# Kernel optimization log

Measured on AMD Instinct MI355X. Metric: run time of the kernel, lower is better.

The kernel has to match this reference:

```python
import jax, jax.numpy as jnp
import numpy as np

N_USERS = 100_000
N_ITEMS = 200_000
N_EDGES = 1_000_000
D = 64        # in_size == every layer_size
L = 3         # number of NGCF layers
B = 4096      # BPR batch
SLOPE = 0.2   # LeakyReLU negative slope
EPS = 1e-12   # F.normalize eps


def setup_inputs() -> dict:
    key = jax.random.key(0)
    ks = jax.random.split(key, 11)
    s = 1.0 / np.sqrt(D)  # xavier-ish scale
    return dict(
        user_feat=jax.random.normal(ks[0], (N_USERS, D), jnp.float32) * s,
        item_feat=jax.random.normal(ks[1], (N_ITEMS, D), jnp.float32) * s,
        W1=jax.random.normal(ks[2], (L, D, D), jnp.float32) * s,
        b1=jnp.zeros((L, D), jnp.float32),
        W2=jax.random.normal(ks[3], (L, D, D), jnp.float32) * s,
        b2=jnp.zeros((L, D), jnp.float32),
        edge_src=jax.random.randint(ks[4], (N_EDGES,), 0, N_USERS),
        edge_dst=jax.random.randint(ks[5], (N_EDGES,), 0, N_ITEMS),
        users=jax.random.randint(ks[6], (B,), 0, N_USERS),
        pos_items=jax.random.randint(ks[7], (B,), 0, N_ITEMS),
        neg_items=jax.random.randint(ks[8], (B,), 0, N_ITEMS),
    )


def _act_norm(h):
    # LeakyReLU(0.2) -> (dropout=identity, eval) -> row-wise L2 normalize
    h = jax.nn.leaky_relu(h, SLOPE)
    n = jnp.linalg.norm(h, axis=1, keepdims=True)
    return h / jnp.maximum(n, EPS)


def _ngcf_forward(user_feat, item_feat, W1, b1, W2, b2, edge_src, edge_dst):
    ones = jnp.ones((edge_src.shape[0],), user_feat.dtype)
    deg_u = jax.ops.segment_sum(ones, edge_src, num_segments=N_USERS)  # out-degree of users
    deg_i = jax.ops.segment_sum(ones, edge_dst, num_segments=N_ITEMS)  # in-degree of items
    norm = (deg_u[edge_src] * deg_i[edge_dst]) ** -0.5  # [E], same for both directions
    norm = norm[:, None]

    hu, hi = user_feat, item_feat
    u_embeds, i_embeds = [hu], [hi]
    for l in range(L):
        # per-edge elementwise product term (shared between both directions)
        p = hu[edge_src] * hi[edge_dst]            # [E, D]
        pw = p @ W2[l] + b2[l]                     # [E, D]
        # user -> item messages, summed per item
        m_i = norm * ((hu @ W1[l] + b1[l])[edge_src] + pw)
        # item -> user messages, summed per user
        m_u = norm * ((hi @ W1[l] + b1[l])[edge_dst] + pw)
        hi_new = jax.ops.segment_sum(m_i, edge_dst, num_segments=N_ITEMS)
        hu_new = jax.ops.segment_sum(m_u, edge_src, num_segments=N_USERS)
        hu, hi = _act_norm(hu_new), _act_norm(hi_new)
        u_embeds.append(hu)
        i_embeds.append(hi)

    user_embd = jnp.concatenate(u_embeds, axis=1)  # [N_USERS, D*(L+1)]
    item_embd = jnp.concatenate(i_embeds, axis=1)  # [N_ITEMS, D*(L+1)]
    return user_embd, item_embd


def reference(user_feat, item_feat, W1, b1, W2, b2,
              edge_src, edge_dst, users, pos_items, neg_items):
    user_embd, item_embd = _ngcf_forward(
        user_feat, item_feat, W1, b1, W2, b2, edge_src, edge_dst)
    return (user_embd[users], item_embd[pos_items], item_embd[neg_items])
```

## Files before the change

kernel.cpp:

```cpp
#include <hip/hip_runtime.h>

#define NU 100000
#define NI 200000
#define NE 1000000
#define NB 4096
#define CAP 16384
#define NBS 98
#define NBD 98
#define NTI (NI / 16)
#define NTU (NU / 16)
#define DBKT 64
#define CAPD 65536
#define NBI 196
#define NBU 98

typedef __attribute__((ext_vector_type(8))) short bf16x8;
typedef __attribute__((ext_vector_type(4))) float f32x4;
typedef __attribute__((ext_vector_type(8))) unsigned short u16x8;

static __device__ __forceinline__ short f2bf(float f) {
  unsigned u = __builtin_bit_cast(unsigned, f);
  unsigned r = (u + 0x7fffu + ((u >> 16) & 1u)) >> 16;
  return (short)r;
}
static __device__ __forceinline__ float bf2f(unsigned short u) {
  return __builtin_bit_cast(float, ((unsigned)u) << 16);
}

__global__ __launch_bounds__(256) void binA_kernel(const int* __restrict__ src,
                                                   const int* __restrict__ dst,
                                                   int* __restrict__ gcur_s,
                                                   int* __restrict__ gcur_d,
                                                   int2* __restrict__ temp_s,
                                                   int2* __restrict__ temp_d) {
  __shared__ int lh[128], lbase[128], lpos[128];
  const int dir = blockIdx.x >> 9;
  const int cb = blockIdx.x & 511;
  const int lo = (int)(((long long)NE * cb) >> 9);
  const int hi = (int)(((long long)NE * (cb + 1)) >> 9);
  const int* key = dir ? dst : src;
  const int* oth = dir ? src : dst;
  int* gcur = dir ? gcur_d : gcur_s;
  int2* temp = dir ? temp_d : temp_s;
  const int shift = dir ? 11 : 10;
  const int tid = threadIdx.x;
  if (tid < 128) lh[tid] = 0;
  __syncthreads();
  for (int e = lo + tid; e < hi; e += 256) atomicAdd(&lh[key[e] >> shift], 1);
  __syncthreads();
  if (tid < 128) {
    const int c = lh[tid];
    lbase[tid] = c ? atomicAdd(&gcur[tid], c) : 0;
    lpos[tid] = 0;
  }
  __syncthreads();
  for (int e = lo + tid; e < hi; e += 256) {
    const int k = key[e];
    const int b = k >> shift;
    const int p = lbase[b] + atomicAdd(&lpos[b], 1);
    temp[(size_t)b * CAP + p] = make_int2(k, oth[e]);
  }
}

__global__ void bktscan_kernel(const int* __restrict__ gcur_s, const int* __restrict__ gcur_d,
                               int* __restrict__ bktofs_s, int* __restrict__ bktofs_d,
                               int* __restrict__ ofs_u, int* __restrict__ ofs_i) {
  const int t = threadIdx.x;
  if (t == 0) {
    int a = 0;
    for (int i = 0; i < NBS; ++i) { bktofs_s[i] = a; a += gcur_s[i]; }
    bktofs_s[NBS] = a;
    ofs_u[NU] = NE;
  }
  if (t == 1) {
    int a = 0;
    for (int i = 0; i < NBD; ++i) { bktofs_d[i] = a; a += gcur_d[i]; }
    bktofs_d[NBD] = a;
    ofs_i[NI] = NE;
  }
}

__global__ __launch_bounds__(256) void placeB_kernel(const int2* __restrict__ temp_s,
                                                     const int2* __restrict__ temp_d,
                                                     const int* __restrict__ gcur_s,
                                                     const int* __restrict__ gcur_d,
                                                     const int* __restrict__ bktofs_s,
                                                     const int* __restrict__ bktofs_d,
                                                     int* __restrict__ ofs_u, int* __restrict__ ofs_i,
                                                     int* __restrict__ by_src, int* __restrict__ by_dst) {
  __shared__ int cnt[2048];
  __shared__ int exc[2048];
  __shared__ int wsum[256];
  const bool isdst = blockIdx.x >= NBS;
  const int b = isdst ? (int)blockIdx.x - NBS : (int)blockIdx.x;
  const int shift = isdst ? 11 : 10;
  const int nodelo = b << shift;
  const int n = isdst ? NI : NU;
  const int2* temp = (isdst ? temp_d : temp_s) + (size_t)b * CAP;
  const int ecnt = (isdst ? gcur_d : gcur_s)[b];
  const int bbase = (isdst ? bktofs_d : bktofs_s)[b];
  int* ofs = isdst ? ofs_i : ofs_u;
  int* by = isdst ? by_dst : by_src;
  const int tid = threadIdx.x;
  const int NN = 1 << shift;

  for (int j = tid; j < NN; j += 256) cnt[j] = 0;
  __syncthreads();
  for (int k = tid; k < ecnt; k += 256) atomicAdd(&cnt[temp[k].x - nodelo], 1);
  __syncthreads();
  const int per = NN >> 8;
  int s = 0;
  for (int j = 0; j < per; ++j) s += cnt[tid * per + j];
  wsum[tid] = s;
  __syncthreads();
  for (int off = 1; off < 256; off <<= 1) {
    int t2 = (tid >= off) ? wsum[tid - off] : 0;
    __syncthreads();
    wsum[tid] += t2;
    __syncthreads();
  }
  int run = wsum[tid] - s;
  for (int j = 0; j < per; ++j) {
    const int idx = tid * per + j;
    exc[idx] = run;
    run += cnt[idx];
  }
  __syncthreads();
  for (int j = tid; j < NN; j += 256) {
    const int node = nodelo + j;
    if (node < n) ofs[node] = bbase + exc[j];
  }
  __syncthreads();
  for (int j = tid; j < NN; j += 256) cnt[j] = exc[j];
  __syncthreads();
  for (int k = tid; k < ecnt; k += 256) {
    const int2 t2 = temp[k];
    const int p = bbase + atomicAdd(&cnt[t2.x - nodelo], 1);
    by[p] = t2.y;
  }
}

__global__ __launch_bounds__(256) void dbinA_kernel(const int* __restrict__ ofs_i,
                                                    const int* __restrict__ ofs_u,
                                                    int* __restrict__ dgcur,
                                                    int* __restrict__ arena_i,
                                                    int* __restrict__ arena_u) {
  __shared__ int lh[DBKT], lbase[DBKT], lpos[DBKT];
  const bool item = blockIdx.x < NBI;
  const int b = item ? (int)blockIdx.x : (int)blockIdx.x - NBI;
  const int n = item ? NI : NU;
  const int* ofs = item ? ofs_i : ofs_u;
  int* cur = dgcur + (item ? 0 : DBKT);
  int* arena = item ? arena_i : arena_u;
  const int nodelo = b << 10;
  const int nodehi = min(nodelo + 1024, n);
  const int tid = threadIdx.x;
  if (tid < DBKT) lh[tid] = 0;
  __syncthreads();
  for (int node = nodelo + tid; node < nodehi; node += 256)
    atomicAdd(&lh[min(ofs[node + 1] - ofs[node], DBKT - 1)], 1);
  __syncthreads();
  if (tid < DBKT) {
    const int c = lh[tid];
    lbase[tid] = c ? atomicAdd(&cur[tid], c) : 0;
    lpos[tid] = 0;
  }
  __syncthreads();
  for (int node = nodelo + tid; node < nodehi; node += 256) {
    const int d = min(ofs[node + 1] - ofs[node], DBKT - 1);
    const int p = lbase[d] + atomicAdd(&lpos[d], 1);
    arena[d * CAPD + p] = node;
  }
}

__global__ void dbktscan_kernel(const int* __restrict__ dgcur,
                                int* __restrict__ dofs, int* __restrict__ dedge,
                                int* __restrict__ ofs2_i, int* __restrict__ ofs2_u) {
  const int t = threadIdx.x;
  if (t == 0) {
    int a = 0, e = 0;
    for (int d = 0; d < DBKT; ++d) { dofs[d] = a; dedge[d] = e; a += dgcur[d]; e += dgcur[d] * d; }
    ofs2_i[NI] = NE;
  }
  if (t == 1) {
    int a = 0, e = 0;
    for (int d = 0; d < DBKT; ++d) {
      dofs[DBKT + d] = a; dedge[DBKT + d] = e;
      a += dgcur[DBKT + d]; e += dgcur[DBKT + d] * d;
    }
    ofs2_u[NU] = NE;
  }
}

__global__ __launch_bounds__(256) void dcompact_kernel(const int* __restrict__ dgcur,
                                                       const int* __restrict__ dofs,
                                                       const int* __restrict__ dedge,
                                                       const int* __restrict__ arena_i,
                                                       const int* __restrict__ arena_u,
                                                       int* __restrict__ perm_i, int* __restrict__ perm_u,
                                                       int* __restrict__ inv_i, int* __restrict__ inv_u,
                                                       int* __restrict__ ofs2_i, int* __restrict__ ofs2_u,
                                                       float* __restrict__ rs2_i, float* __restrict__ rs2_u,
                                                       float* __restrict__ srs2_i, float* __restrict__ srs2_u) {
  const int bk = blockIdx.x;
  const bool item = bk < DBKT;
  const int d = item ? bk : bk - DBKT;
  const int cnt = dgcur[bk];
  const int nodebase = dofs[bk];
  const int edgebase = dedge[bk];
  const int* arena = item ? arena_i : arena_u;
  int* perm = item ? perm_i : perm_u;
  int* inv = item ? inv_i : inv_u;
  int* ofs2 = item ? ofs2_i : ofs2_u;
  float* rs2 = item ? rs2_i : rs2_u;
  float* srs2 = item ? srs2_i : srs2_u;
  const float rsv = d ? rsqrtf((float)d) : 0.f;
  const float srsv = d ? sqrtf((float)d) : 0.f;
  for (int k = threadIdx.x; k < cnt; k += 256) {
    const int node = arena[d * CAPD + k];
    const int r = nodebase + k;
    perm[r] = node;
    inv[node] = r;
    ofs2[r] = edgebase + k * d;
    rs2[r] = rsv;
    srs2[r] = srsv;
  }
}

__global__ __launch_bounds__(256) void remapby_kernel(const int* __restrict__ ofs_i,
                                                      const int* __restrict__ ofs_u,
                                                      const int* __restrict__ ofs2_i,
                                                      const int* __restrict__ ofs2_u,
                                                      const int* __restrict__ perm_i,
                                                      const int* __restrict__ perm_u,
                                                      const int* __restrict__ inv_i,
                                                      const int* __restrict__ inv_u,
                                                      const int* __restrict__ by_dst,
                                                      const int* __restrict__ by_src,
                                                      int* __restrict__ by2_dst,
                                                      int* __restrict__ by2_src) {
  int r = blockIdx.x * 256 + threadIdx.x;
  if (r < NI) {
    const int lo2 = ofs2_i[r];
    const int d = ofs2_i[r + 1] - lo2;
    const int oo = ofs_i[perm_i[r]];
    for (int k = 0; k < d; ++k) by2_dst[lo2 + k] = inv_u[by_dst[oo + k]];
  } else if (r < NI + NU) {
    r -= NI;
    const int lo2 = ofs2_u[r];
    const int d = ofs2_u[r + 1] - lo2;
    const int oo = ofs_u[perm_u[r]];
    for (int k = 0; k < d; ++k) by2_src[lo2 + k] = inv_i[by_src[oo + k]];
  }
}

__global__ __launch_bounds__(256) void c_kernel(const int* __restrict__ ofs2_i,
                                                const int* __restrict__ ofs2_u,
                                                const int* __restrict__ by2_dst,
                                                const int* __restrict__ by2_src,
                                                const float* __restrict__ rs2_u,
                                                const float* __restrict__ rs2_i,
                                                float* __restrict__ c_i,
                                                float* __restrict__ c_u) {
  int r = blockIdx.x * 256 + threadIdx.x;
  if (r < NI) {
    const int lo = ofs2_i[r], hi = ofs2_i[r + 1];
    float s = 0.f;
    for (int k = lo; k < hi; ++k) s += rs2_u[by2_dst[k]];
    c_i[r] = rs2_i[r] * s;
  } else if (r < NI + NU) {
    r -= NI;
    const int lo = ofs2_u[r], hi = ofs2_u[r + 1];
    float s = 0.f;
    for (int k = lo; k < hi; ++k) s += rs2_i[by2_src[k]];
    c_u[r] = rs2_u[r] * s;
  }
}

__global__ __launch_bounds__(256) void conv_kernel(const float* __restrict__ uf,
                                                   const float* __restrict__ itf,
                                                   const int* __restrict__ perm_u,
                                                   const int* __restrict__ perm_i,
                                                   const float* __restrict__ rs2_u,
                                                   const float* __restrict__ rs2_i,
                                                   unsigned short* __restrict__ hsu,
                                                   unsigned short* __restrict__ hsi) {
  int i = blockIdx.x * 256 + threadIdx.x;
  const int n4u = NU * 16;
  const float* in;
  const int* perm;
  const float* rs;
  unsigned short* outp;
  int j;
  if (i < n4u) {
    in = uf; perm = perm_u; rs = rs2_u; outp = hsu; j = i;
  } else if (i < n4u + NI * 16) {
    in = itf; perm = perm_i; rs = rs2_i; outp = hsi; j = i - n4u;
  } else return;
  const int rnew = j >> 4;
  const int grp = j & 15;
  const float rsn = rs[rnew];
  float4 v = *(const float4*)&in[(size_t)perm[rnew] * 64 + grp * 4];
  ushort4 o;
  o.x = (unsigned short)f2bf(v.x * rsn);
  o.y = (unsigned short)f2bf(v.y * rsn);
  o.z = (unsigned short)f2bf(v.z * rsn);
  o.w = (unsigned short)f2bf(v.w * rsn);
  *(ushort4*)&outp[(size_t)j * 4] = o;
}

__global__ __launch_bounds__(256) void layer_fused_kernel(const int* __restrict__ ofs2_i,
                                                          const int* __restrict__ ofs2_u,
                                                          const int* __restrict__ by2_dst,
                                                          const int* __restrict__ by2_src,
                                                          const float* __restrict__ rs2_u,
                                                          const float* __restrict__ rs2_i,
                                                          const float* __restrict__ c_i,
                                                          const float* __restrict__ c_u,
                                                          const unsigned short* __restrict__ hsu,
                                                          const unsigned short* __restrict__ hsi,
                                                          const float* __restrict__ W1,
                                                          const float* __restrict__ b1,
                                                          const float* __restrict__ W2,
                                                          const float* __restrict__ b2,
                                                          unsigned short* __restrict__ hsi_new,
                                                          unsigned short* __restrict__ hsu_new) {
  __shared__ unsigned short wlds[8192];
  const int tid = threadIdx.x;
  const int lane = tid & 63;
  const int row16 = lane & 15;
  const int kg = lane >> 4;
  for (int ch = tid; ch < 1024; ch += 256) {
    const int w = ch >> 9;
    const int rem = ch & 511;
    const int nb = rem >> 7, kb = (rem >> 6) & 1, l2 = rem & 63;
    const int r16 = l2 & 15, kg2 = l2 >> 4;
    const float* W = w ? W2 : W1;
    unsigned short* dstp = &wlds[ch * 8];
#pragma unroll
    for (int j = 0; j < 8; ++j)
      dstp[j] = (unsigned short)f2bf(W[(kb * 32 + kg2 * 8 + j) * 64 + nb * 16 + r16]);
  }
  __syncthreads();

  float bsum[4];
#pragma unroll
  for (int nb = 0; nb < 4; ++nb) bsum[nb] = b1[nb * 16 + row16] + b2[nb * 16 + row16];

  const int wid = (blockIdx.x * 256 + tid) >> 6;
  const int nwaves = (gridDim.x * 256) >> 6;

  for (int t = wid; t < NTI + NTU; t += nwaves) {
    const bool item = t < NTI;
    const int tt = item ? t : t - NTI;
    const int* ofs = item ? ofs2_i : ofs2_u;
    const int* pay = item ? by2_dst : by2_src;
    const float* rsw = item ? rs2_i : rs2_u;
    const float* cc = item ? c_i : c_u;
    const unsigned short* hs = item ? hsu : hsi;
    const unsigned short* hsown = item ? hsi : hsu;
    unsigned short* hsnew = item ? hsi_new : hsu_new;
    const int r0 = tt * 16;
    const int node = r0 + row16;

    const int lo = ofs[node], hiE = ofs[node + 1];
    int rounds = (hiE - lo + 3) >> 2;
#pragma unroll
    for (int m = 1; m < 16; m <<= 1) rounds = max(rounds, __shfl_xor(rounds, m));

    float a0[8] = {0.f, 0.f, 0.f, 0.f, 0.f, 0.f, 0.f, 0.f};
    float a1[8] = {0.f, 0.f, 0.f, 0.f, 0.f, 0.f, 0.f, 0.f};
    for (int rd = 0; rd < rounds; ++rd) {
      const int i0 = lo + rd * 4;
      int nb4[4];
      float wt[4];
#pragma unroll
      for (int s = 0; s < 4; ++s) {
        const int idx = i0 + s;
        nb4[s] = pay[min(idx, NE - 1)];
        wt[s] = (idx < hiE) ? 1.f : 0.f;
      }
      u16x8 h0[4], h1[4];
#pragma unroll
      for (int s = 0; s < 4; ++s) {
        const unsigned short* hp = hs + (size_t)nb4[s] * 64 + kg * 8;
        h0[s] = *(const u16x8*)hp;
        h1[s] = *(const u16x8*)(hp + 32);
      }
#pragma unroll
      for (int s = 0; s < 4; ++s)
#pragma unroll
        for (int j = 0; j < 8; ++j) {
          a0[j] += wt[s] * bf2f(h0[s][j]);
          a1[j] += wt[s] * bf2f(h1[s][j]);
        }
    }

    const float rsn = rsw[node];
    const float cnode = cc[node];
    const unsigned short* hp = hsown + (size_t)node * 64 + kg * 8;
    const u16x8 hv0 = *(const u16x8*)hp;
    const u16x8 hv1 = *(const u16x8*)(hp + 32);
    bf16x8 ag[2], ap[2];
#pragma unroll
    for (int j = 0; j < 8; ++j) {
      ag[0][j] = f2bf(a0[j] * rsn);
      ag[1][j] = f2bf(a1[j] * rsn);
      ap[0][j] = f2bf(a0[j] * bf2f(hv0[j]));
      ap[1][j] = f2bf(a1[j] * bf2f(hv1[j]));
    }

    f32x4 acc[4];
#pragma unroll
    for (int nb = 0; nb < 4; ++nb) acc[nb] = (f32x4){0.f, 0.f, 0.f, 0.f};
    const unsigned short* wl = wlds + lane * 8;
#pragma unroll
    for (int nb = 0; nb < 4; ++nb)
#pragma unroll
      for (int kb = 0; kb < 2; ++kb) {
        const bf16x8 w1f = *(const bf16x8*)(wl + ((0 * 4 + nb) * 2 + kb) * 512);
        const bf16x8 w2f = *(const bf16x8*)(wl + ((1 * 4 + nb) * 2 + kb) * 512);
        acc[nb] = __builtin_amdgcn_mfma_f32_16x16x32_bf16(ag[kb], w1f, acc[nb], 0, 0, 0);
        acc[nb] = __builtin_amdgcn_mfma_f32_16x16x32_bf16(ap[kb], w2f, acc[nb], 0, 0, 0);
      }

    float cv[4], rsrow[4];
#pragma unroll
    for (int reg = 0; reg < 4; ++reg) {
      cv[reg] = __shfl(cnode, kg * 4 + reg);
      rsrow[reg] = __shfl(rsn, kg * 4 + reg);
    }
    float v[4][4];
    float ss[4] = {0.f, 0.f, 0.f, 0.f};
#pragma unroll
    for (int nb = 0; nb < 4; ++nb)
#pragma unroll
      for (int reg = 0; reg < 4; ++reg) {
        float x = acc[nb][reg] + cv[reg] * bsum[nb];
        x = (x > 0.f) ? x : 0.2f * x;
        v[nb][reg] = x;
        ss[reg] += x * x;
      }
#pragma unroll
    for (int m = 1; m < 16; m <<= 1)
#pragma unroll
      for (int reg = 0; reg < 4; ++reg) ss[reg] += __shfl_xor(ss[reg], m);
#pragma unroll
    for (int reg = 0; reg < 4; ++reg) {
      const float invs = rsrow[reg] / fmaxf(sqrtf(ss[reg]), 1e-12f);
      const size_t rowbase = (size_t)(r0 + kg * 4 + reg) * 64;
#pragma unroll
      for (int nb = 0; nb < 4; ++nb)
        hsnew[rowbase + nb * 16 + row16] = (unsigned short)f2bf(v[nb][reg] * invs);
    }
  }
}

__global__ __launch_bounds__(256) void gather_f32_kernel(const float* __restrict__ hu,
                                                         const float* __restrict__ hi,
                                                         const int* __restrict__ users,
                                                         const int* __restrict__ pos,
                                                         const int* __restrict__ neg,
                                                         float* __restrict__ out) {
  int t = blockIdx.x * 256 + threadIdx.x;
  if (t >= 3 * NB * 64) return;
  int j = t & 63;
  int b = (t >> 6) & (NB - 1);
  int which = t / (NB * 64);
  int row = (which == 0) ? users[b] : ((which == 1) ? pos[b] : neg[b]);
  const float* h = (which == 0) ? hu : hi;
  out[(size_t)which * NB * 256 + (size_t)b * 256 + j] = h[(size_t)row * 64 + j];
}

__global__ __launch_bounds__(256) void gather_bf_kernel(const unsigned short* __restrict__ hsu,
                                                        const unsigned short* __restrict__ hsi,
                                                        const float* __restrict__ srs2_u,
                                                        const float* __restrict__ srs2_i,
                                                        const int* __restrict__ inv_u,
                                                        const int* __restrict__ inv_i,
                                                        const int* __restrict__ users,
                                                        const int* __restrict__ pos,
                                                        const int* __restrict__ neg,
                                                        float* __restrict__ out, int stage) {
  int t = blockIdx.x * 256 + threadIdx.x;
  if (t >= 3 * NB * 64) return;
  int j = t & 63;
  int b = (t >> 6) & (NB - 1);
  int which = t / (NB * 64);
  int row = (which == 0) ? users[b] : ((which == 1) ? pos[b] : neg[b]);
  const int rnew = (which == 0) ? inv_u[row] : inv_i[row];
  const unsigned short* h = (which == 0) ? hsu : hsi;
  const float s = (which == 0) ? srs2_u[rnew] : srs2_i[rnew];
  out[(size_t)which * NB * 256 + (size_t)b * 256 + (size_t)stage * 64 + j] =
      bf2f(h[(size_t)rnew * 64 + j]) * s;
}

extern "C" void kernel_launch(void* const* d_in, const int* in_sizes, int n_in,
                              void* d_out, int out_size, void* d_ws, size_t ws_size,
                              hipStream_t stream) {
  (void)in_sizes; (void)n_in; (void)out_size; (void)ws_size;
  const float* user_feat = (const float*)d_in[0];
  const float* item_feat = (const float*)d_in[1];
  const float* W1 = (const float*)d_in[2];
  const float* b1 = (const float*)d_in[3];
  const float* W2 = (const float*)d_in[4];
  const float* b2 = (const float*)d_in[5];
  const int* edge_src = (const int*)d_in[6];
  const int* edge_dst = (const int*)d_in[7];
  const int* users = (const int*)d_in[8];
  const int* pos_items = (const int*)d_in[9];
  const int* neg_items = (const int*)d_in[10];
  float* out = (float*)d_out;

  char* base = (char*)d_ws;
  size_t ofsz = 0;
  auto alloc = [&](size_t bytes) -> char* {
    char* r = base + ofsz;
    ofsz += (bytes + 1023) & ~(size_t)1023;
    return r;
  };
  int* ofs_u = (int*)alloc((NU + 1) * 4);
  int* ofs_i = (int*)alloc((NI + 1) * 4);
  int* ofs2_u = (int*)alloc((NU + 1) * 4);
  int* ofs2_i = (int*)alloc((NI + 1) * 4);
  int* gcur_s = (int*)alloc(128 * 4);
  int* gcur_d = (int*)alloc(128 * 4);
  int* bktofs_s = (int*)alloc(128 * 4);
  int* bktofs_d = (int*)alloc(128 * 4);
  int* dgcur = (int*)alloc(2 * DBKT * 4);
  int* dofs = (int*)alloc(2 * DBKT * 4);
  int* dedge = (int*)alloc(2 * DBKT * 4);
  int2* temp_s = (int2*)alloc((size_t)NBS * CAP * 8);
  int2* temp_d = (int2*)alloc((size_t)NBD * CAP * 8);
  int* by_src = (int*)alloc((size_t)NE * 4);
  int* by_dst = (int*)alloc((size_t)NE * 4);
  int* by2_src = (int*)alloc((size_t)NE * 4);
  int* by2_dst = (int*)alloc((size_t)NE * 4);
  int* arena_i = (int*)alloc((size_t)DBKT * CAPD * 4);
  int* arena_u = (int*)alloc((size_t)DBKT * CAPD * 4);
  int* perm_i = (int*)alloc((size_t)NI * 4);
  int* perm_u = (int*)alloc((size_t)NU * 4);
  int* inv_i = (int*)alloc((size_t)NI * 4);
  int* inv_u = (int*)alloc((size_t)NU * 4);
  float* rs2_u = (float*)alloc((size_t)NU * 4);
  float* rs2_i = (float*)alloc((size_t)NI * 4);
  float* srs2_u = (float*)alloc((size_t)NU * 4);
  float* srs2_i = (float*)alloc((size_t)NI * 4);
  float* c_u = (float*)alloc((size_t)NU * 4);
  float* c_i = (float*)alloc((size_t)NI * 4);
  unsigned short* hsU0 = (unsigned short*)alloc((size_t)NU * 64 * 2);
  unsigned short* hsU1 = (unsigned short*)alloc((size_t)NU * 64 * 2);
  unsigned short* hsI0 = (unsigned short*)alloc((size_t)NI * 64 * 2);
  unsigned short* hsI1 = (unsigned short*)alloc((size_t)NI * 64 * 2);

  unsigned short* bufU[2] = {hsU1, hsU0};
  unsigned short* bufI[2] = {hsI1, hsI0};

  hipMemsetAsync(gcur_s, 0, 128 * 4, stream);
  hipMemsetAsync(gcur_d, 0, 128 * 4, stream);
  hipMemsetAsync(dgcur, 0, 2 * DBKT * 4, stream);
  binA_kernel<<<1024, 256, 0, stream>>>(edge_src, edge_dst, gcur_s, gcur_d, temp_s, temp_d);
  bktscan_kernel<<<1, 64, 0, stream>>>(gcur_s, gcur_d, bktofs_s, bktofs_d, ofs_u, ofs_i);
  placeB_kernel<<<NBS + NBD, 256, 0, stream>>>(temp_s, temp_d, gcur_s, gcur_d,
                                               bktofs_s, bktofs_d, ofs_u, ofs_i,
                                               by_src, by_dst);
  dbinA_kernel<<<NBI + NBU, 256, 0, stream>>>(ofs_i, ofs_u, dgcur, arena_i, arena_u);
  dbktscan_kernel<<<1, 64, 0, stream>>>(dgcur, dofs, dedge, ofs2_i, ofs2_u);
  dcompact_kernel<<<2 * DBKT, 256, 0, stream>>>(dgcur, dofs, dedge, arena_i, arena_u,
                                                perm_i, perm_u, inv_i, inv_u,
                                                ofs2_i, ofs2_u, rs2_i, rs2_u, srs2_i, srs2_u);
  remapby_kernel<<<(NI + NU + 255) / 256, 256, 0, stream>>>(ofs_i, ofs_u, ofs2_i, ofs2_u,
                                                            perm_i, perm_u, inv_i, inv_u,
                                                            by_dst, by_src, by2_dst, by2_src);
  c_kernel<<<(NI + NU + 255) / 256, 256, 0, stream>>>(ofs2_i, ofs2_u, by2_dst, by2_src,
                                                      rs2_u, rs2_i, c_i, c_u);
  conv_kernel<<<((NU + NI) * 16 + 255) / 256, 256, 0, stream>>>(
      user_feat, item_feat, perm_u, perm_i, rs2_u, rs2_i, hsU0, hsI0);

  gather_f32_kernel<<<(3 * NB * 64 + 255) / 256, 256, 0, stream>>>(
      user_feat, item_feat, users, pos_items, neg_items, out);

  const unsigned short* hsu = hsU0;
  const unsigned short* hsi = hsI0;
  for (int l = 0; l < 3; ++l) {
    unsigned short* hsu_new = bufU[l & 1];
    unsigned short* hsi_new = bufI[l & 1];
    layer_fused_kernel<<<2048, 256, 0, stream>>>(ofs2_i, ofs2_u, by2_dst, by2_src,
                                                 rs2_u, rs2_i, c_i, c_u,
                                                 hsu, hsi,
                                                 W1 + l * 4096, b1 + l * 64,
                                                 W2 + l * 4096, b2 + l * 64,
                                                 hsi_new, hsu_new);
    gather_bf_kernel<<<(3 * NB * 64 + 255) / 256, 256, 0, stream>>>(
        hsu_new, hsi_new, srs2_u, srs2_i, inv_u, inv_i,
        users, pos_items, neg_items, out, l + 1);
    hsu = hsu_new;
    hsi = hsi_new;
  }
}
```

Baseline: 427.3 us.

## Fuse edge remap and degree-coefficient sum into one edge-parallel kernel

The per-node remap and coefficient kernels, which looped serially over each node's edges, are replaced by one edge-parallel kernel. Each thread binary-searches the degree bucket for its edge position, remaps one neighbour index, and atomically adds the neighbour's rsqrt-degree into a raw per-node sum. The node's own rsqrt factor is now applied in the layer kernel, and the sum buffers are zeroed with memsets. This trades the load imbalance of per-node loops and one kernel launch for per-edge atomics and a short binary search.

```diff
diff --git a/kernel.cpp b/kernel.cpp
--- a/kernel.cpp
+++ b/kernel.cpp
@@ -180,14 +180,16 @@
   if (t == 0) {
     int a = 0, e = 0;
     for (int d = 0; d < DBKT; ++d) { dofs[d] = a; dedge[d] = e; a += dgcur[d]; e += dgcur[d] * d; }
+    dedge[DBKT] = NE;
     ofs2_i[NI] = NE;
   }
   if (t == 1) {
     int a = 0, e = 0;
     for (int d = 0; d < DBKT; ++d) {
-      dofs[DBKT + d] = a; dedge[DBKT + d] = e;
+      dofs[DBKT + d] = a; dedge[65 + d] = e;
       a += dgcur[DBKT + d]; e += dgcur[DBKT + d] * d;
     }
+    dedge[65 + DBKT] = NE;
     ofs2_u[NU] = NE;
   }
 }
@@ -207,7 +209,7 @@
   const int d = item ? bk : bk - DBKT;
   const int cnt = dgcur[bk];
   const int nodebase = dofs[bk];
-  const int edgebase = dedge[bk];
+  const int edgebase = dedge[item ? d : 65 + d];
   const int* arena = item ? arena_i : arena_u;
   int* perm = item ? perm_i : perm_u;
   int* inv = item ? inv_i : inv_u;
@@ -227,54 +229,46 @@
   }
 }
 
-__global__ __launch_bounds__(256) void remapby_kernel(const int* __restrict__ ofs_i,
-                                                      const int* __restrict__ ofs_u,
-                                                      const int* __restrict__ ofs2_i,
-                                                      const int* __restrict__ ofs2_u,
-                                                      const int* __restrict__ perm_i,
-                                                      const int* __restrict__ perm_u,
-                                                      const int* __restrict__ inv_i,
-                                                      const int* __restrict__ inv_u,
-                                                      const int* __restrict__ by_dst,
-                                                      const int* __restrict__ by_src,
-                                                      int* __restrict__ by2_dst,
-                                                      int* __restrict__ by2_src) {
-  int r = blockIdx.x * 256 + threadIdx.x;
-  if (r < NI) {
-    const int lo2 = ofs2_i[r];
-    const int d = ofs2_i[r + 1] - lo2;
-    const int oo = ofs_i[perm_i[r]];
-    for (int k = 0; k < d; ++k) by2_dst[lo2 + k] = inv_u[by_dst[oo + k]];
-  } else if (r < NI + NU) {
-    r -= NI;
-    const int lo2 = ofs2_u[r];
-    const int d = ofs2_u[r + 1] - lo2;
-    const int oo = ofs_u[perm_u[r]];
-    for (int k = 0; k < d; ++k) by2_src[lo2 + k] = inv_i[by_src[oo + k]];
-  }
-}
-
-__global__ __launch_bounds__(256) void c_kernel(const int* __restrict__ ofs2_i,
-                                                const int* __restrict__ ofs2_u,
-                                                const int* __restrict__ by2_dst,
-                                                const int* __restrict__ by2_src,
-                                                const float* __restrict__ rs2_u,
-                                                const float* __restrict__ rs2_i,
-                                                float* __restrict__ c_i,
-                                                float* __restrict__ c_u) {
-  int r = blockIdx.x * 256 + threadIdx.x;
-  if (r < NI) {
-    const int lo = ofs2_i[r], hi = ofs2_i[r + 1];
-    float s = 0.f;
-    for (int k = lo; k < hi; ++k) s += rs2_u[by2_dst[k]];
-    c_i[r] = rs2_i[r] * s;
-  } else if (r < NI + NU) {
-    r -= NI;
-    const int lo = ofs2_u[r], hi = ofs2_u[r + 1];
-    float s = 0.f;
-    for (int k = lo; k < hi; ++k) s += rs2_i[by2_src[k]];
-    c_u[r] = rs2_u[r] * s;
-  }
+__global__ __launch_bounds__(256) void remap2_kernel(const int* __restrict__ dedge,
+                                                     const int* __restrict__ dofs,
+                                                     const int* __restrict__ ofs_i,
+                                                     const int* __restrict__ ofs_u,
+                                                     const int* __restrict__ perm_i,
+                                                     const int* __restrict__ perm_u,
+                                                     const int* __restrict__ inv_i,
+                                                     const int* __restrict__ inv_u,
+                                                     const int* __restrict__ by_dst,
+                                                     const int* __restrict__ by_src,
+                                                     const float* __restrict__ rs2_u,
+                                                     const float* __restrict__ rs2_i,
+                                                     int* __restrict__ by2_dst,
+                                                     int* __restrict__ by2_src,
+                                                     float* __restrict__ craw_i,
+                                                     float* __restrict__ craw_u) {
+  __shared__ int de[65];
+  const int t = blockIdx.x * 256 + threadIdx.x;
+  const bool item = blockIdx.x < (NE + 255) / 256;
+  if (threadIdx.x < 65) de[threadIdx.x] = dedge[item ? threadIdx.x : 65 + threadIdx.x];
+  __syncthreads();
+  const int pos = item ? t : t - ((NE + 255) / 256) * 256;
+  if (pos >= NE) return;
+
+  int lo = 0, hi = 64;
+  while (hi - lo > 1) {
+    const int mid = (lo + hi) >> 1;
+    if (de[mid] <= pos) lo = mid; else hi = mid;
+  }
+  const int d = lo;
+  const int idx = pos - de[d];
+  const int nrank = idx / d;
+  const int k = idx - nrank * d;
+  const int node = dofs[item ? d : DBKT + d] + nrank;
+  const int orig = (item ? perm_i : perm_u)[node];
+  const int oo = (item ? ofs_i : ofs_u)[orig];
+  const int v = (item ? by_dst : by_src)[oo + k];
+  const int nv = (item ? inv_u : inv_i)[v];
+  (item ? by2_dst : by2_src)[pos] = nv;
+  atomicAdd(&(item ? craw_i : craw_u)[node], (item ? rs2_u : rs2_i)[nv]);
 }
 
 __global__ __launch_bounds__(256) void conv_kernel(const float* __restrict__ uf,
@@ -315,8 +309,8 @@
                                                           const int* __restrict__ by2_src,
                                                           const float* __restrict__ rs2_u,
                                                           const float* __restrict__ rs2_i,
-                                                          const float* __restrict__ c_i,
-                                                          const float* __restrict__ c_u,
+                                                          const float* __restrict__ craw_i,
+                                                          const float* __restrict__ craw_u,
                                                           const unsigned short* __restrict__ hsu,
                                                           const unsigned short* __restrict__ hsi,
                                                           const float* __restrict__ W1,
@@ -356,7 +350,7 @@
     const int* ofs = item ? ofs2_i : ofs2_u;
     const int* pay = item ? by2_dst : by2_src;
     const float* rsw = item ? rs2_i : rs2_u;
-    const float* cc = item ? c_i : c_u;
+    const float* cc = item ? craw_i : craw_u;
     const unsigned short* hs = item ? hsu : hsi;
     const unsigned short* hsown = item ? hsi : hsu;
     unsigned short* hsnew = item ? hsi_new : hsu_new;
@@ -397,7 +391,7 @@
     }
 
     const float rsn = rsw[node];
-    const float cnode = cc[node];
+    const float cnode = cc[node] * rsn;
     const unsigned short* hp = hsown + (size_t)node * 64 + kg * 8;
     const u16x8 hv0 = *(const u16x8*)hp;
     const u16x8 hv1 = *(const u16x8*)(hp + 32);
@@ -529,7 +523,7 @@
   int* bktofs_d = (int*)alloc(128 * 4);
   int* dgcur = (int*)alloc(2 * DBKT * 4);
   int* dofs = (int*)alloc(2 * DBKT * 4);
-  int* dedge = (int*)alloc(2 * DBKT * 4);
+  int* dedge = (int*)alloc(2 * 65 * 4);
   int2* temp_s = (int2*)alloc((size_t)NBS * CAP * 8);
   int2* temp_d = (int2*)alloc((size_t)NBD * CAP * 8);
   int* by_src = (int*)alloc((size_t)NE * 4);
@@ -546,8 +540,8 @@
   float* rs2_i = (float*)alloc((size_t)NI * 4);
   float* srs2_u = (float*)alloc((size_t)NU * 4);
   float* srs2_i = (float*)alloc((size_t)NI * 4);
-  float* c_u = (float*)alloc((size_t)NU * 4);
-  float* c_i = (float*)alloc((size_t)NI * 4);
+  float* craw_u = (float*)alloc((size_t)NU * 4);
+  float* craw_i = (float*)alloc((size_t)NI * 4);
   unsigned short* hsU0 = (unsigned short*)alloc((size_t)NU * 64 * 2);
   unsigned short* hsU1 = (unsigned short*)alloc((size_t)NU * 64 * 2);
   unsigned short* hsI0 = (unsigned short*)alloc((size_t)NI * 64 * 2);
@@ -559,6 +553,8 @@
   hipMemsetAsync(gcur_s, 0, 128 * 4, stream);
   hipMemsetAsync(gcur_d, 0, 128 * 4, stream);
   hipMemsetAsync(dgcur, 0, 2 * DBKT * 4, stream);
+  hipMemsetAsync(craw_u, 0, (size_t)NU * 4, stream);
+  hipMemsetAsync(craw_i, 0, (size_t)NI * 4, stream);
   binA_kernel<<<1024, 256, 0, stream>>>(edge_src, edge_dst, gcur_s, gcur_d, temp_s, temp_d);
   bktscan_kernel<<<1, 64, 0, stream>>>(gcur_s, gcur_d, bktofs_s, bktofs_d, ofs_u, ofs_i);
   placeB_kernel<<<NBS + NBD, 256, 0, stream>>>(temp_s, temp_d, gcur_s, gcur_d,
@@ -569,11 +565,11 @@
   dcompact_kernel<<<2 * DBKT, 256, 0, stream>>>(dgcur, dofs, dedge, arena_i, arena_u,
                                                 perm_i, perm_u, inv_i, inv_u,
                                                 ofs2_i, ofs2_u, rs2_i, rs2_u, srs2_i, srs2_u);
-  remapby_kernel<<<(NI + NU + 255) / 256, 256, 0, stream>>>(ofs_i, ofs_u, ofs2_i, ofs2_u,
-                                                            perm_i, perm_u, inv_i, inv_u,
-                                                            by_dst, by_src, by2_dst, by2_src);
-  c_kernel<<<(NI + NU + 255) / 256, 256, 0, stream>>>(ofs2_i, ofs2_u, by2_dst, by2_src,
-                                                      rs2_u, rs2_i, c_i, c_u);
+  const int halfgrid = (NE + 255) / 256;
+  remap2_kernel<<<2 * halfgrid, 256, 0, stream>>>(dedge, dofs, ofs_i, ofs_u,
+                                                  perm_i, perm_u, inv_i, inv_u,
+                                                  by_dst, by_src, rs2_u, rs2_i,
+                                                  by2_dst, by2_src, craw_i, craw_u);
   conv_kernel<<<((NU + NI) * 16 + 255) / 256, 256, 0, stream>>>(
       user_feat, item_feat, perm_u, perm_i, rs2_u, rs2_i, hsU0, hsI0);
 
@@ -586,7 +582,7 @@
     unsigned short* hsu_new = bufU[l & 1];
     unsigned short* hsi_new = bufI[l & 1];
     layer_fused_kernel<<<2048, 256, 0, stream>>>(ofs2_i, ofs2_u, by2_dst, by2_src,
-                                                 rs2_u, rs2_i, c_i, c_u,
+                                                 rs2_u, rs2_i, craw_i, craw_u,
                                                  hsu, hsi,
                                                  W1 + l * 4096, b1 + l * 64,
                                                  W2 + l * 4096, b2 + l * 64,
```

Result: slower. 493.1 us (+15.4%).

## Fuse remap with coefficient pass and write batch outputs from layer kernel

Applied to the files above, without the earlier changes.

Merges the edge-index remap and the per-node coefficient sum into one kernel, so the remapped neighbor list is not written and then read back. Removes the per-layer bf16 gather kernel: a linked list built once maps each graph node to the batch slots that request it, and the fused layer kernel writes fp32 normalized rows straight into the output. This also outputs unquantized values instead of bf16-rounded ones. It adds a per-row head lookup and a serial list walk in the layer epilogue, plus uncoalesced scattered writes for hot nodes. The dedge layout is also reshaped to hold end sentinels.

```diff
diff --git a/kernel.cpp b/kernel.cpp
--- a/kernel.cpp
+++ b/kernel.cpp
@@ -180,14 +180,16 @@
   if (t == 0) {
     int a = 0, e = 0;
     for (int d = 0; d < DBKT; ++d) { dofs[d] = a; dedge[d] = e; a += dgcur[d]; e += dgcur[d] * d; }
+    dedge[DBKT] = NE;
     ofs2_i[NI] = NE;
   }
   if (t == 1) {
     int a = 0, e = 0;
     for (int d = 0; d < DBKT; ++d) {
-      dofs[DBKT + d] = a; dedge[DBKT + d] = e;
+      dofs[DBKT + d] = a; dedge[65 + d] = e;
       a += dgcur[DBKT + d]; e += dgcur[DBKT + d] * d;
     }
+    dedge[65 + DBKT] = NE;
     ofs2_u[NU] = NE;
   }
 }
@@ -200,22 +202,19 @@
                                                        int* __restrict__ perm_i, int* __restrict__ perm_u,
                                                        int* __restrict__ inv_i, int* __restrict__ inv_u,
                                                        int* __restrict__ ofs2_i, int* __restrict__ ofs2_u,
-                                                       float* __restrict__ rs2_i, float* __restrict__ rs2_u,
-                                                       float* __restrict__ srs2_i, float* __restrict__ srs2_u) {
+                                                       float* __restrict__ rs2_i, float* __restrict__ rs2_u) {
   const int bk = blockIdx.x;
   const bool item = bk < DBKT;
   const int d = item ? bk : bk - DBKT;
   const int cnt = dgcur[bk];
   const int nodebase = dofs[bk];
-  const int edgebase = dedge[bk];
+  const int edgebase = dedge[item ? d : 65 + d];
   const int* arena = item ? arena_i : arena_u;
   int* perm = item ? perm_i : perm_u;
   int* inv = item ? inv_i : inv_u;
   int* ofs2 = item ? ofs2_i : ofs2_u;
   float* rs2 = item ? rs2_i : rs2_u;
-  float* srs2 = item ? srs2_i : srs2_u;
   const float rsv = d ? rsqrtf((float)d) : 0.f;
-  const float srsv = d ? sqrtf((float)d) : 0.f;
   for (int k = threadIdx.x; k < cnt; k += 256) {
     const int node = arena[d * CAPD + k];
     const int r = nodebase + k;
@@ -223,58 +222,77 @@
     inv[node] = r;
     ofs2[r] = edgebase + k * d;
     rs2[r] = rsv;
-    srs2[r] = srsv;
-  }
-}
-
-__global__ __launch_bounds__(256) void remapby_kernel(const int* __restrict__ ofs_i,
-                                                      const int* __restrict__ ofs_u,
-                                                      const int* __restrict__ ofs2_i,
-                                                      const int* __restrict__ ofs2_u,
-                                                      const int* __restrict__ perm_i,
-                                                      const int* __restrict__ perm_u,
-                                                      const int* __restrict__ inv_i,
-                                                      const int* __restrict__ inv_u,
-                                                      const int* __restrict__ by_dst,
-                                                      const int* __restrict__ by_src,
-                                                      int* __restrict__ by2_dst,
-                                                      int* __restrict__ by2_src) {
+  }
+}
+
+__global__ __launch_bounds__(256) void remap3_kernel(const int* __restrict__ ofs_i,
+                                                     const int* __restrict__ ofs_u,
+                                                     const int* __restrict__ ofs2_i,
+                                                     const int* __restrict__ ofs2_u,
+                                                     const int* __restrict__ perm_i,
+                                                     const int* __restrict__ perm_u,
+                                                     const int* __restrict__ inv_i,
+                                                     const int* __restrict__ inv_u,
+                                                     const int* __restrict__ by_dst,
+                                                     const int* __restrict__ by_src,
+                                                     const float* __restrict__ rs2_u,
+                                                     const float* __restrict__ rs2_i,
+                                                     int* __restrict__ by2_dst,
+                                                     int* __restrict__ by2_src,
+                                                     float* __restrict__ c_i,
+                                                     float* __restrict__ c_u) {
   int r = blockIdx.x * 256 + threadIdx.x;
+  const int *ofs, *ofs2, *perm, *invo, *by;
+  const float *rso, *rsw;
+  int* by2;
+  float* c;
+  int rr;
   if (r < NI) {
-    const int lo2 = ofs2_i[r];
-    const int d = ofs2_i[r + 1] - lo2;
-    const int oo = ofs_i[perm_i[r]];
-    for (int k = 0; k < d; ++k) by2_dst[lo2 + k] = inv_u[by_dst[oo + k]];
+    rr = r; ofs = ofs_i; ofs2 = ofs2_i; perm = perm_i; invo = inv_u;
+    by = by_dst; rso = rs2_u; rsw = rs2_i; by2 = by2_dst; c = c_i;
   } else if (r < NI + NU) {
-    r -= NI;
-    const int lo2 = ofs2_u[r];
-    const int d = ofs2_u[r + 1] - lo2;
-    const int oo = ofs_u[perm_u[r]];
-    for (int k = 0; k < d; ++k) by2_src[lo2 + k] = inv_i[by_src[oo + k]];
-  }
-}
-
-__global__ __launch_bounds__(256) void c_kernel(const int* __restrict__ ofs2_i,
-                                                const int* __restrict__ ofs2_u,
-                                                const int* __restrict__ by2_dst,
-                                                const int* __restrict__ by2_src,
-                                                const float* __restrict__ rs2_u,
-                                                const float* __restrict__ rs2_i,
-                                                float* __restrict__ c_i,
-                                                float* __restrict__ c_u) {
-  int r = blockIdx.x * 256 + threadIdx.x;
-  if (r < NI) {
-    const int lo = ofs2_i[r], hi = ofs2_i[r + 1];
-    float s = 0.f;
-    for (int k = lo; k < hi; ++k) s += rs2_u[by2_dst[k]];
-    c_i[r] = rs2_i[r] * s;
-  } else if (r < NI + NU) {
-    r -= NI;
-    const int lo = ofs2_u[r], hi = ofs2_u[r + 1];
-    float s = 0.f;
-    for (int k = lo; k < hi; ++k) s += rs2_i[by2_src[k]];
-    c_u[r] = rs2_u[r] * s;
-  }
+    rr = r - NI; ofs = ofs_u; ofs2 = ofs2_u; perm = perm_u; invo = inv_i;
+    by = by_src; rso = rs2_i; rsw = rs2_u; by2 = by2_src; c = c_u;
+  } else return;
+  const int lo2 = ofs2[rr];
+  const int d = ofs2[rr + 1] - lo2;
+  float sum = 0.f;
+  if (d > 0) {
+    const int oo = ofs[perm[rr]];
+    for (int k0 = 0; k0 < d; k0 += 4) {
+      int v4[4], nv[4];
+#pragma unroll
+      for (int s = 0; s < 4; ++s) v4[s] = by[oo + min(k0 + s, d - 1)];
+#pragma unroll
+      for (int s = 0; s < 4; ++s) nv[s] = invo[v4[s]];
+#pragma unroll
+      for (int s = 0; s < 4; ++s)
+        if (k0 + s < d) {
+          by2[lo2 + k0 + s] = nv[s];
+          sum += rso[nv[s]];
+        }
+    }
+  }
+  c[rr] = rsw[rr] * sum;
+}
+
+__global__ __launch_bounds__(256) void obuild_kernel(const int* __restrict__ users,
+                                                     const int* __restrict__ pos,
+                                                     const int* __restrict__ neg,
+                                                     const int* __restrict__ inv_u,
+                                                     const int* __restrict__ inv_i,
+                                                     int* __restrict__ head_u,
+                                                     int* __restrict__ head_i,
+                                                     int* __restrict__ nxt) {
+  const int s = blockIdx.x * 256 + threadIdx.x;
+  if (s >= 3 * NB) return;
+  const int which = s / NB, b = s - which * NB;
+  const int row = (which == 0) ? users[b] : ((which == 1) ? pos[b] : neg[b]);
+  int node;
+  int* head;
+  if (which == 0) { node = inv_u[row]; head = head_u; }
+  else            { node = inv_i[row]; head = head_i; }
+  nxt[s] = atomicExch(&head[node], s);
 }
 
 __global__ __launch_bounds__(256) void conv_kernel(const float* __restrict__ uf,
@@ -323,6 +341,11 @@
                                                           const float* __restrict__ b1,
                                                           const float* __restrict__ W2,
                                                           const float* __restrict__ b2,
+                                                          const int* __restrict__ head_i,
+                                                          const int* __restrict__ head_u,
+                                                          const int* __restrict__ nxt,
+                                                          float* __restrict__ outp,
+                                                          int stage,
                                                           unsigned short* __restrict__ hsi_new,
                                                           unsigned short* __restrict__ hsu_new) {
   __shared__ unsigned short wlds[8192];
@@ -357,6 +380,7 @@
     const int* pay = item ? by2_dst : by2_src;
     const float* rsw = item ? rs2_i : rs2_u;
     const float* cc = item ? c_i : c_u;
+    const int* head = item ? head_i : head_u;
     const unsigned short* hs = item ? hsu : hsi;
     const unsigned short* hsown = item ? hsi : hsu;
     unsigned short* hsnew = item ? hsi_new : hsu_new;
@@ -447,11 +471,20 @@
       for (int reg = 0; reg < 4; ++reg) ss[reg] += __shfl_xor(ss[reg], m);
 #pragma unroll
     for (int reg = 0; reg < 4; ++reg) {
-      const float invs = rsrow[reg] / fmaxf(sqrtf(ss[reg]), 1e-12f);
-      const size_t rowbase = (size_t)(r0 + kg * 4 + reg) * 64;
+      const int noder = r0 + kg * 4 + reg;
+      const float invn = 1.0f / fmaxf(sqrtf(ss[reg]), 1e-12f);
+      const float invs = invn * rsrow[reg];
+      const size_t rowbase = (size_t)noder * 64;
 #pragma unroll
       for (int nb = 0; nb < 4; ++nb)
         hsnew[rowbase + nb * 16 + row16] = (unsigned short)f2bf(v[nb][reg] * invs);
+      int s = head[noder];
+      while (s >= 0) {
+        float* op = outp + (size_t)s * 256 + stage * 64;
+#pragma unroll
+        for (int nb = 0; nb < 4; ++nb) op[nb * 16 + row16] = v[nb][reg] * invn;
+        s = nxt[s];
+      }
     }
   }
 }
@@ -470,29 +503,6 @@
   int row = (which == 0) ? users[b] : ((which == 1) ? pos[b] : neg[b]);
   const float* h = (which == 0) ? hu : hi;
   out[(size_t)which * NB * 256 + (size_t)b * 256 + j] = h[(size_t)row * 64 + j];
-}
-
-__global__ __launch_bounds__(256) void gather_bf_kernel(const unsigned short* __restrict__ hsu,
-                                                        const unsigned short* __restrict__ hsi,
-                                                        const float* __restrict__ srs2_u,
-                                                        const float* __restrict__ srs2_i,
-                                                        const int* __restrict__ inv_u,
-                                                        const int* __restrict__ inv_i,
-                                                        const int* __restrict__ users,
-                                                        const int* __restrict__ pos,
-                                                        const int* __restrict__ neg,
-                                                        float* __restrict__ out, int stage) {
-  int t = blockIdx.x * 256 + threadIdx.x;
-  if (t >= 3 * NB * 64) return;
-  int j = t & 63;
-  int b = (t >> 6) & (NB - 1);
-  int which = t / (NB * 64);
-  int row = (which == 0) ? users[b] : ((which == 1) ? pos[b] : neg[b]);
-  const int rnew = (which == 0) ? inv_u[row] : inv_i[row];
-  const unsigned short* h = (which == 0) ? hsu : hsi;
-  const float s = (which == 0) ? srs2_u[rnew] : srs2_i[rnew];
-  out[(size_t)which * NB * 256 + (size_t)b * 256 + (size_t)stage * 64 + j] =
-      bf2f(h[(size_t)rnew * 64 + j]) * s;
 }
 
 extern "C" void kernel_launch(void* const* d_in, const int* in_sizes, int n_in,
@@ -529,7 +539,7 @@
   int* bktofs_d = (int*)alloc(128 * 4);
   int* dgcur = (int*)alloc(2 * DBKT * 4);
   int* dofs = (int*)alloc(2 * DBKT * 4);
-  int* dedge = (int*)alloc(2 * DBKT * 4);
+  int* dedge = (int*)alloc(2 * 65 * 4);
   int2* temp_s = (int2*)alloc((size_t)NBS * CAP * 8);
   int2* temp_d = (int2*)alloc((size_t)NBD * CAP * 8);
   int* by_src = (int*)alloc((size_t)NE * 4);
@@ -544,10 +554,11 @@
   int* inv_u = (int*)alloc((size_t)NU * 4);
   float* rs2_u = (float*)alloc((size_t)NU * 4);
   float* rs2_i = (float*)alloc((size_t)NI * 4);
-  float* srs2_u = (float*)alloc((size_t)NU * 4);
-  float* srs2_i = (float*)alloc((size_t)NI * 4);
   float* c_u = (float*)alloc((size_t)NU * 4);
   float* c_i = (float*)alloc((size_t)NI * 4);
+  int* head_u = (int*)alloc((size_t)NU * 4);
+  int* head_i = (int*)alloc((size_t)NI * 4);
+  int* onxt = (int*)alloc(3 * NB * 4);
   unsigned short* hsU0 = (unsigned short*)alloc((size_t)NU * 64 * 2);
   unsigned short* hsU1 = (unsigned short*)alloc((size_t)NU * 64 * 2);
   unsigned short* hsI0 = (unsigned short*)alloc((size_t)NI * 64 * 2);
@@ -559,6 +570,8 @@
   hipMemsetAsync(gcur_s, 0, 128 * 4, stream);
   hipMemsetAsync(gcur_d, 0, 128 * 4, stream);
   hipMemsetAsync(dgcur, 0, 2 * DBKT * 4, stream);
+  hipMemsetAsync(head_u, 0xFF, (size_t)NU * 4, stream);
+  hipMemsetAsync(head_i, 0xFF, (size_t)NI * 4, stream);
   binA_kernel<<<1024, 256, 0, stream>>>(edge_src, edge_dst, gcur_s, gcur_d, temp_s, temp_d);
   bktscan_kernel<<<1, 64, 0, stream>>>(gcur_s, gcur_d, bktofs_s, bktofs_d, ofs_u, ofs_i);
   placeB_kernel<<<NBS + NBD, 256, 0, stream>>>(temp_s, temp_d, gcur_s, gcur_d,
@@ -568,12 +581,13 @@
   dbktscan_kernel<<<1, 64, 0, stream>>>(dgcur, dofs, dedge, ofs2_i, ofs2_u);
   dcompact_kernel<<<2 * DBKT, 256, 0, stream>>>(dgcur, dofs, dedge, arena_i, arena_u,
                                                 perm_i, perm_u, inv_i, inv_u,
-                                                ofs2_i, ofs2_u, rs2_i, rs2_u, srs2_i, srs2_u);
-  remapby_kernel<<<(NI + NU + 255) / 256, 256, 0, stream>>>(ofs_i, ofs_u, ofs2_i, ofs2_u,
-                                                            perm_i, perm_u, inv_i, inv_u,
-                                                            by_dst, by_src, by2_dst, by2_src);
-  c_kernel<<<(NI + NU + 255) / 256, 256, 0, stream>>>(ofs2_i, ofs2_u, by2_dst, by2_src,
-                                                      rs2_u, rs2_i, c_i, c_u);
+                                                ofs2_i, ofs2_u, rs2_i, rs2_u);
+  remap3_kernel<<<(NI + NU + 255) / 256, 256, 0, stream>>>(ofs_i, ofs_u, ofs2_i, ofs2_u,
+                                                           perm_i, perm_u, inv_i, inv_u,
+                                                           by_dst, by_src, rs2_u, rs2_i,
+                                                           by2_dst, by2_src, c_i, c_u);
+  obuild_kernel<<<(3 * NB + 255) / 256, 256, 0, stream>>>(users, pos_items, neg_items,
+                                                          inv_u, inv_i, head_u, head_i, onxt);
   conv_kernel<<<((NU + NI) * 16 + 255) / 256, 256, 0, stream>>>(
       user_feat, item_feat, perm_u, perm_i, rs2_u, rs2_i, hsU0, hsI0);
 
@@ -590,10 +604,8 @@
                                                  hsu, hsi,
                                                  W1 + l * 4096, b1 + l * 64,
                                                  W2 + l * 4096, b2 + l * 64,
+                                                 head_i, head_u, onxt, out, l + 1,
                                                  hsi_new, hsu_new);
-    gather_bf_kernel<<<(3 * NB * 64 + 255) / 256, 256, 0, stream>>>(
-        hsu_new, hsi_new, srs2_u, srs2_i, inv_u, inv_i,
-        users, pos_items, neg_items, out, l + 1);
     hsu = hsu_new;
     hsi = hsi_new;
   }
```

Measured after the change: 434.8 us. No clear change (+1.8%).
